# Performance work log

Hardware: AMD Instinct MI355X
Metric: run time of the kernel (lower is better)

Reference implementation:

```python
import jax, jax.numpy as jnp
import numpy as np

SELU_SCALE = 1.0507009873554805
SELU_ALPHA = 1.6732632423543772

def _learned_activation(x, w):
    # softmax-blended mixture of 8 activations plus a zero 'linear' branch
    p = jax.nn.softmax(w)
    sig = jax.nn.sigmoid(x)
    elu = jax.nn.elu(x)
    tanh = jnp.tanh(x)
    relu = jax.nn.relu(x)
    silu = jax.nn.silu(x)
    gelu = jax.nn.gelu(x, approximate=False)
    selu = SELU_SCALE * jnp.where(x > 0, x, SELU_ALPHA * jnp.expm1(x))
    mish = x * jnp.tanh(jax.nn.softplus(x))
    return (p[0] * sig + p[1] * elu + p[2] * tanh + p[3] * relu
            + p[4] * silu + p[5] * gelu + p[6] * selu + p[7] * mish)  # p[8]*0 (linear=0)


def setup_inputs() -> dict:
    key = jax.random.key(0)
    ks = jax.random.split(key, 10)
    B, D, H, E, M = 1024, 1024, 2048, 8, 2048
    init_units = 1024
    s = lambda fan_in: 1.0 / np.sqrt(fan_in)
    x = jax.random.normal(ks[0], (B, D), jnp.float32)
    gate_w = jax.random.normal(ks[1], (D, E), jnp.float32) * s(D)
    expert_w = jax.random.normal(ks[2], (E, D, H), jnp.float32) * s(D)
    expert_b = jnp.zeros((E, H), jnp.float32)
    conn_w1 = jax.random.normal(ks[3], (E, H, 32), jnp.float32) * s(H)
    conn_b1 = jnp.zeros((E, 32), jnp.float32)
    conn_w2 = jax.random.normal(ks[4], (E, 32, H), jnp.float32) * s(32)
    conn_b2 = jnp.zeros((E, H), jnp.float32)
    neuron_avg = jax.random.uniform(ks[5], (E, H), jnp.float32)
    # initial mask: first initial_units neurons active per expert
    neuron_mask = jnp.tile(
        jnp.concatenate([jnp.ones((init_units,), jnp.float32),
                         jnp.zeros((H - init_units,), jnp.float32)])[None, :], (E, 1))
    mem_read_w = jax.random.normal(ks[6], (H, M), jnp.float32) * s(H)
    mem_read_b = jnp.zeros((M,), jnp.float32)
    memory = jax.random.normal(ks[7], (M, H), jnp.float32) * s(M)
    act_w = jnp.ones((9,), jnp.float32)
    return {"x": x, "gate_w": gate_w, "expert_w": expert_w, "expert_b": expert_b,
            "conn_w1": conn_w1, "conn_b1": conn_b1, "conn_w2": conn_w2, "conn_b2": conn_b2,
            "neuron_avg": neuron_avg, "neuron_mask": neuron_mask,
            "mem_read_w": mem_read_w, "mem_read_b": mem_read_b,
            "memory": memory, "act_w": act_w}


def reference(x, gate_w, expert_w, expert_b, conn_w1, conn_b1, conn_w2, conn_b2,
              neuron_avg, neuron_mask, mem_read_w, mem_read_b, memory, act_w):
    # --- MoE gate over experts ---
    gate = jax.nn.softmax(x @ gate_w, axis=-1)  # [B, E]
    # --- DynamicConnectivity soft gating, per expert (from neuron_activation_avg) ---
    h1 = jax.nn.relu(jnp.einsum('eh,ehk->ek', neuron_avg, conn_w1) + conn_b1)  # [E, 32]
    conn = jax.nn.sigmoid(jnp.einsum('ek,ekh->eh', h1, conn_w2) + conn_b2)     # [E, H]
    # --- plastic dense experts: z -> gated -> masked -> relu ---
    z = jnp.einsum('bd,edh->ebh', x, expert_w) + expert_b[:, None, :]  # [E, B, H]
    a = jax.nn.relu(z * (conn * neuron_mask)[:, None, :])              # [E, B, H]
    moe_out = jnp.einsum('be,ebh->bh', gate, a)                        # [B, H]
    # --- episodic memory read (attention over memory slots) ---
    attn = jax.nn.softmax(moe_out @ mem_read_w + mem_read_b, axis=-1)  # [B, M]
    read_vec = attn @ memory                                           # [B, H]
    # --- blended learned activation on residual sum ---
    return _learned_activation(moe_out + read_vec, act_w)
```

## Files before the change

kernel.cpp:

```cpp
#include <hip/hip_runtime.h>
#include <hip/hip_bf16.h>
#include <math.h>

typedef __bf16 bf16_t;
typedef __bf16 bf16x8 __attribute__((ext_vector_type(8)));
typedef float f32x4 __attribute__((ext_vector_type(4)));

#define B_DIM 1024
#define D_DIM 1024
#define H_DIM 2048
#define E_DIM 8
#define M_DIM 2048

typedef const __attribute__((address_space(1))) unsigned int as1_uint;
typedef __attribute__((address_space(3))) unsigned int as3_uint;

__device__ __forceinline__ void gl_lds16(const void* g, void* l) {
  __builtin_amdgcn_global_load_lds((as1_uint*)g, (as3_uint*)l, 16, 0, 0);
}

#define WAITV(n) asm volatile("s_waitcnt vmcnt(" #n ")" ::: "memory")

__global__ __launch_bounds__(256) void cvt_kernel(const float* __restrict__ in,
                                                  bf16_t* __restrict__ out) {
  size_t i = ((size_t)blockIdx.x * 256 + threadIdx.x) * 8;
  float4 a = *(const float4*)&in[i];
  float4 b = *(const float4*)&in[i + 4];
  bf16x8 o;
  o[0] = (bf16_t)a.x; o[1] = (bf16_t)a.y; o[2] = (bf16_t)a.z; o[3] = (bf16_t)a.w;
  o[4] = (bf16_t)b.x; o[5] = (bf16_t)b.y; o[6] = (bf16_t)b.z; o[7] = (bf16_t)b.w;
  *(bf16x8*)&out[i] = o;
}

__global__ __launch_bounds__(256) void transpose_all(
    const float* __restrict__ ew, const float* __restrict__ mrw, const float* __restrict__ mem,
    bf16_t* __restrict__ wbT, bf16_t* __restrict__ mrT, bf16_t* __restrict__ memT) {
  __shared__ float tile[64][65];
  const int z = blockIdx.z;
  const float* in; bf16_t* out; int R, C;
  if (z < 8) {
    if (blockIdx.y >= 16) return;
    in = ew + (size_t)z * D_DIM * H_DIM; out = wbT + (size_t)z * D_DIM * H_DIM;
    R = D_DIM; C = H_DIM;
  } else if (z == 8) {
    in = mrw; out = mrT; R = H_DIM; C = M_DIM;
  } else {
    in = mem; out = memT; R = M_DIM; C = H_DIM;
  }
  int c0 = blockIdx.x * 64, r0 = blockIdx.y * 64;
  int t = threadIdx.x;
  int cq = (t & 15) * 4, rr = t >> 4;
#pragma unroll
  for (int i = 0; i < 4; ++i) {
    int r = rr + 16 * i;
    float4 v = *(const float4*)&in[(size_t)(r0 + r) * C + c0 + cq];
    tile[r][cq] = v.x; tile[r][cq + 1] = v.y; tile[r][cq + 2] = v.z; tile[r][cq + 3] = v.w;
  }
  __syncthreads();
  int r8 = (t & 7) * 8, cc = t >> 3;
#pragma unroll
  for (int i = 0; i < 2; ++i) {
    int c = cc + 32 * i;
    bf16x8 o;
#pragma unroll
    for (int j = 0; j < 8; ++j) o[j] = (bf16_t)tile[r8 + j][c];
    *(bf16x8*)&out[(size_t)(c0 + c) * R + r0 + r8] = o;
  }
}

__global__ __launch_bounds__(256) void gate_kernel(
    const float* __restrict__ x, const float* __restrict__ gw, float* __restrict__ gate_t) {
  __shared__ float red[256][8];
  int b = blockIdx.x, t = threadIdx.x;
  float acc[8] = {0.f, 0.f, 0.f, 0.f, 0.f, 0.f, 0.f, 0.f};
  for (int d = t; d < D_DIM; d += 256) {
    float xv = x[(size_t)b * D_DIM + d];
#pragma unroll
    for (int e = 0; e < 8; ++e) acc[e] += xv * gw[d * 8 + e];
  }
#pragma unroll
  for (int e = 0; e < 8; ++e) red[t][e] = acc[e];
  __syncthreads();
  for (int s = 128; s > 0; s >>= 1) {
    if (t < s) {
#pragma unroll
      for (int e = 0; e < 8; ++e) red[t][e] += red[t + s][e];
    }
    __syncthreads();
  }
  if (t == 0) {
    float m = red[0][0];
#pragma unroll
    for (int e = 1; e < 8; ++e) m = fmaxf(m, red[0][e]);
    float p[8], sum = 0.f;
#pragma unroll
    for (int e = 0; e < 8; ++e) { p[e] = expf(red[0][e] - m); sum += p[e]; }
    float inv = 1.f / sum;
#pragma unroll
    for (int e = 0; e < 8; ++e) gate_t[e * B_DIM + b] = p[e] * inv;
  }
}

__global__ __launch_bounds__(256) void conn1_kernel(
    const float* __restrict__ avg, const float* __restrict__ w1, float* __restrict__ h1p) {
  __shared__ float red[256 * 32];
  int e = blockIdx.x >> 3, c = blockIdx.x & 7, t = threadIdx.x;
  int h = c * 256 + t;
  float av = avg[e * H_DIM + h];
  const float* w1p = &w1[((size_t)e * H_DIM + h) * 32];
#pragma unroll
  for (int k = 0; k < 32; ++k) red[t * 32 + k] = av * w1p[k];
  __syncthreads();
  for (int s = 128; s > 0; s >>= 1) {
    if (t < s) {
#pragma unroll
      for (int k = 0; k < 32; ++k) red[t * 32 + k] += red[(t + s) * 32 + k];
    }
    __syncthreads();
  }
  if (t < 32) h1p[(e * 8 + c) * 32 + t] = red[t];
}

__global__ __launch_bounds__(256) void conn2_kernel(
    const float* __restrict__ h1p, const float* __restrict__ b1,
    const float* __restrict__ w2, const float* __restrict__ b2,
    const float* __restrict__ mask, float* __restrict__ conn) {
  __shared__ float h1[32];
  int e = blockIdx.x >> 3, c = blockIdx.x & 7, t = threadIdx.x;
  if (t < 32) {
    float s = 0.f;
#pragma unroll
    for (int c2 = 0; c2 < 8; ++c2) s += h1p[(e * 8 + c2) * 32 + t];
    h1[t] = fmaxf(s + b1[e * 32 + t], 0.f);
  }
  __syncthreads();
  int h = c * 256 + t;
  float s = b2[e * H_DIM + h];
#pragma unroll
  for (int k = 0; k < 32; ++k) s += h1[k] * w2[((size_t)e * 32 + k) * H_DIM + h];
  conn[e * H_DIM + h] = (1.f / (1.f + expf(-s))) * mask[e * H_DIM + h];
}

__global__ __launch_bounds__(512, 2) void expert_gemm(
    const bf16_t* __restrict__ A, const bf16_t* __restrict__ Bt,
    float* __restrict__ moe, bf16_t* __restrict__ moebf,
    const float* __restrict__ gate_t, const float* __restrict__ conn,
    const float* __restrict__ ebias) {
  __shared__ bf16_t As[2][128 * 64];
  __shared__ bf16_t Bs[8][64 * 64];

  const int wid = (blockIdx.x & 7) * 32 + (blockIdx.x >> 3);
  const int b0 = (wid & 7) * 128;
  const int n0 = (wid >> 3) * 64;

  const int t = threadIdx.x;
  const int lane = t & 63, wave = t >> 6;
  const int wmh = wave >> 2, wnq = wave & 3;
  const int lr = lane & 15, lk = (lane >> 4) * 8;
  const int csw = (lr & 7) << 3;
  const int srow = lane >> 3;
  const int scol = ((lane & 7) ^ srow) << 3;
  const size_t EB = (size_t)H_DIM * D_DIM;

  const bf16_t* Asrc = A + (size_t)(b0 + wave * 16 + srow) * D_DIM + scol;
  const bf16_t* Bsrc = Bt + (size_t)(n0 + wave * 8 + srow) * D_DIM + scol;

  auto stageA = [&](int buf, int kt) {
    gl_lds16(Asrc + (size_t)kt * 64, &As[buf][(wave * 16) * 64]);
    gl_lds16(Asrc + 8 * D_DIM + (size_t)kt * 64, &As[buf][(wave * 16 + 8) * 64]);
  };
  auto stageB = [&](int slot, int e, int kt) {
    gl_lds16(Bsrc + (size_t)e * EB + (size_t)kt * 64, &Bs[slot][(wave * 8) * 64]);
  };
  auto readB = [&](int slot, bf16x8& r0, bf16x8& r1) {
    const bf16_t* Bb = &Bs[slot][0];
    r0 = *(const bf16x8*)&Bb[(wnq * 16 + lr) * 64 + (lk ^ csw)];
    r1 = *(const bf16x8*)&Bb[(wnq * 16 + lr) * 64 + ((32 + lk) ^ csw)];
  };

  f32x4 acc[8][4];
#pragma unroll
  for (int e = 0; e < 8; ++e)
#pragma unroll
    for (int mf = 0; mf < 4; ++mf) acc[e][mf] = (f32x4){0.f, 0.f, 0.f, 0.f};

  stageA(0, 0);
  stageB(0, 0, 0);
  stageB(1, 1, 0);
  stageB(2, 2, 0);
  stageB(3, 3, 0);

  for (int kt = 0; kt < 16; ++kt) {
    const int ab = kt & 1;
    const bool last = (kt == 15);
    bf16x8 af[2][4];
#pragma unroll
    for (int eh = 0; eh < 4; ++eh) {
      const int e0 = eh * 2, e1 = e0 + 1;
      if (eh < 2) {
        stageB(e0 + 4, e0 + 4, kt);
        stageB(e1 + 4, e1 + 4, kt);
      } else if (!last) {
        stageB(e0 - 4, e0 - 4, kt + 1);
        stageB(e1 - 4, e1 - 4, kt + 1);
        if (eh == 2) stageA(ab ^ 1, kt + 1);
      }
      if (eh < 2)        { WAITV(4); }
      else if (!last)    { WAITV(6); }
      else if (eh == 2)  { WAITV(2); }
      else               { WAITV(0); }
      __builtin_amdgcn_s_barrier();
      __builtin_amdgcn_sched_barrier(0);
      if (eh == 0) {
#pragma unroll
        for (int kk = 0; kk < 2; ++kk)
#pragma unroll
          for (int mf = 0; mf < 4; ++mf)
            af[kk][mf] = *(const bf16x8*)&As[ab][(wmh * 64 + mf * 16 + lr) * 64 +
                                                ((kk * 32 + lk) ^ csw)];
      }
      bf16x8 p0, p1, q0, q1;
      readB(e0, p0, p1);
      readB(e1, q0, q1);
      __builtin_amdgcn_s_setprio(1);
#pragma unroll
      for (int mf = 0; mf < 4; ++mf) {
        acc[e0][mf] = __builtin_amdgcn_mfma_f32_16x16x32_bf16(af[0][mf], p0, acc[e0][mf], 0, 0, 0);
        acc[e0][mf] = __builtin_amdgcn_mfma_f32_16x16x32_bf16(af[1][mf], p1, acc[e0][mf], 0, 0, 0);
      }
#pragma unroll
      for (int mf = 0; mf < 4; ++mf) {
        acc[e1][mf] = __builtin_amdgcn_mfma_f32_16x16x32_bf16(af[0][mf], q0, acc[e1][mf], 0, 0, 0);
        acc[e1][mf] = __builtin_amdgcn_mfma_f32_16x16x32_bf16(af[1][mf], q1, acc[e1][mf], 0, 0, 0);
      }
      __builtin_amdgcn_s_setprio(0);
    }
  }

  const int r4 = (lane >> 4) * 4;
  const int gcol = n0 + wnq * 16 + lr;
  const int growb = b0 + wmh * 64;
  f32x4 sum[4];
#pragma unroll
  for (int mf = 0; mf < 4; ++mf) sum[mf] = (f32x4){0.f, 0.f, 0.f, 0.f};
#pragma unroll
  for (int e = 0; e < 8; ++e) {
    const float cm = conn[e * H_DIM + gcol];
    const float bb = ebias[e * H_DIM + gcol];
#pragma unroll
    for (int mf = 0; mf < 4; ++mf) {
      const float4 g4 = *(const float4*)&gate_t[e * B_DIM + growb + mf * 16 + r4];
      sum[mf][0] += fmaxf((acc[e][mf][0] + bb) * cm, 0.f) * g4.x;
      sum[mf][1] += fmaxf((acc[e][mf][1] + bb) * cm, 0.f) * g4.y;
      sum[mf][2] += fmaxf((acc[e][mf][2] + bb) * cm, 0.f) * g4.z;
      sum[mf][3] += fmaxf((acc[e][mf][3] + bb) * cm, 0.f) * g4.w;
    }
  }
#pragma unroll
  for (int mf = 0; mf < 4; ++mf)
#pragma unroll
    for (int j = 0; j < 4; ++j) {
      const int grow = growb + mf * 16 + r4 + j;
      moe[(size_t)grow * H_DIM + gcol] = sum[mf][j];
      moebf[(size_t)grow * H_DIM + gcol] = (bf16_t)sum[mf][j];
    }
}

__global__ __launch_bounds__(512, 2) void gemm_sk4(
    const bf16_t* __restrict__ A, const bf16_t* __restrict__ Bt, float* __restrict__ C) {
  __shared__ bf16_t As[2][128 * 64];
  __shared__ bf16_t Bs[2][128 * 64];

  const int wid = (blockIdx.x & 7) * 64 + (blockIdx.x >> 3);
  const int ez = wid >> 7;
  const int rem = wid & 127;
  const int b0 = (rem & 7) * 128;
  const int n0 = (rem >> 3) * 128;
  const int kbase = ez << 9;

  const int t = threadIdx.x;
  const int lane = t & 63, wave = t >> 6;
  const int wm = wave >> 2, wn = wave & 3;
  const int lr = lane & 15, lk = (lane >> 4) * 8;
  const int csw = (lr & 7) << 3;
  const int srow = lane >> 3;
  const int scol = ((lane & 7) ^ srow) << 3;

  const bf16_t* Arow = A + (size_t)(b0 + srow) * 2048 + kbase + scol;
  const bf16_t* Brow = Bt + (size_t)(n0 + srow) * 2048 + kbase + scol;

  const f32x4 zv = {0.f, 0.f, 0.f, 0.f};
  f32x4 acc[4][2];
#pragma unroll
  for (int mf = 0; mf < 4; ++mf)
#pragma unroll
    for (int nf = 0; nf < 2; ++nf) acc[mf][nf] = zv;

  auto STAGE = [&](int bsel, int kt) {
    const int ko = kt << 6;
#pragma unroll
    for (int i = 0; i < 2; ++i) {
      int rb = i * 64 + wave * 8;
      gl_lds16(Arow + (size_t)rb * 2048 + ko, &As[bsel][rb * 64]);
      gl_lds16(Brow + (size_t)rb * 2048 + ko, &Bs[bsel][rb * 64]);
    }
  };

  auto COMPUTE = [&](int bsel) {
    bf16x8 bfr[2][2];
#pragma unroll
    for (int kk = 0; kk < 2; ++kk)
#pragma unroll
      for (int nf = 0; nf < 2; ++nf)
        bfr[kk][nf] = *(const bf16x8*)&Bs[bsel][(wn * 32 + nf * 16 + lr) * 64 + ((kk * 32 + lk) ^ csw)];
    __builtin_amdgcn_s_setprio(1);
#pragma unroll
    for (int mf = 0; mf < 4; ++mf) {
      bf16x8 a0 = *(const bf16x8*)&As[bsel][(wm * 64 + mf * 16 + lr) * 64 + (lk ^ csw)];
      bf16x8 a1 = *(const bf16x8*)&As[bsel][(wm * 64 + mf * 16 + lr) * 64 + ((32 + lk) ^ csw)];
#pragma unroll
      for (int nf = 0; nf < 2; ++nf)
        acc[mf][nf] = __builtin_amdgcn_mfma_f32_16x16x32_bf16(a0, bfr[0][nf], acc[mf][nf], 0, 0, 0);
#pragma unroll
      for (int nf = 0; nf < 2; ++nf)
        acc[mf][nf] = __builtin_amdgcn_mfma_f32_16x16x32_bf16(a1, bfr[1][nf], acc[mf][nf], 0, 0, 0);
    }
    __builtin_amdgcn_s_setprio(0);
  };

  STAGE(0, 0);
  __syncthreads();
  for (int kt = 0; kt < 7; ++kt) {
    STAGE((kt + 1) & 1, kt + 1);
    COMPUTE(kt & 1);
    __syncthreads();
  }
  COMPUTE(1);

  const int r4 = (lane >> 4) * 4;
#pragma unroll
  for (int mf = 0; mf < 4; ++mf) {
#pragma unroll
    for (int nf = 0; nf < 2; ++nf) {
      int gcol = n0 + wn * 32 + nf * 16 + lr;
#pragma unroll
      for (int j = 0; j < 4; ++j) {
        int grow = b0 + wm * 64 + mf * 16 + r4 + j;
        C[((size_t)ez * B_DIM + grow) * 2048 + gcol] = acc[mf][nf][j];
      }
    }
  }
}

__global__ __launch_bounds__(256) void softmax_kernel(
    const float* __restrict__ lg, const float* __restrict__ bias, bf16_t* __restrict__ attn) {
  const size_t P = (size_t)B_DIM * M_DIM;
  int b = blockIdx.x, t = threadIdx.x;
  int lane = t & 63, wave = t >> 6;
  __shared__ float rmax[4], rsum[4];
  float v[8];
  float m = -1e30f;
#pragma unroll
  for (int i = 0; i < 8; ++i) {
    size_t idx = (size_t)b * M_DIM + i * 256 + t;
    v[i] = lg[idx] + lg[P + idx] + lg[2 * P + idx] + lg[3 * P + idx] + bias[i * 256 + t];
    m = fmaxf(m, v[i]);
  }
#pragma unroll
  for (int off = 32; off >= 1; off >>= 1) m = fmaxf(m, __shfl_xor(m, off));
  if (lane == 0) rmax[wave] = m;
  __syncthreads();
  m = fmaxf(fmaxf(rmax[0], rmax[1]), fmaxf(rmax[2], rmax[3]));
  float s = 0.f;
#pragma unroll
  for (int i = 0; i < 8; ++i) {
    v[i] = __expf(v[i] - m);
    s += v[i];
  }
#pragma unroll
  for (int off = 32; off >= 1; off >>= 1) s += __shfl_xor(s, off);
  if (lane == 0) rsum[wave] = s;
  __syncthreads();
  s = rsum[0] + rsum[1] + rsum[2] + rsum[3];
  float inv = 1.f / s;
#pragma unroll
  for (int i = 0; i < 8; ++i) attn[(size_t)b * M_DIM + i * 256 + t] = (bf16_t)(v[i] * inv);
}

__global__ __launch_bounds__(256) void act_kernel(
    const float* __restrict__ rdv, const float* __restrict__ aw, float* __restrict__ out) {
  const size_t P = (size_t)B_DIM * H_DIM;
  int i = blockIdx.x * 256 + threadIdx.x;
  float w[9], m = -1e30f;
#pragma unroll
  for (int j = 0; j < 9; ++j) { w[j] = aw[j]; m = fmaxf(m, w[j]); }
  float p[9], s = 0.f;
#pragma unroll
  for (int j = 0; j < 9; ++j) { p[j] = expf(w[j] - m); s += p[j]; }
  float inv = 1.f / s;
#pragma unroll
  for (int j = 0; j < 9; ++j) p[j] *= inv;
  float4 mv = ((const float4*)out)[i];
  float4 r0 = ((const float4*)rdv)[i];
  float4 r1 = ((const float4*)(rdv + P))[i];
  float4 r2 = ((const float4*)(rdv + 2 * P))[i];
  float4 r3 = ((const float4*)(rdv + 3 * P))[i];
  float xs[4] = {mv.x + r0.x + r1.x + r2.x + r3.x, mv.y + r0.y + r1.y + r2.y + r3.y,
                 mv.z + r0.z + r1.z + r2.z + r3.z, mv.w + r0.w + r1.w + r2.w + r3.w};
  float os[4];
#pragma unroll
  for (int q = 0; q < 4; ++q) {
    float xv = xs[q];
    float enx = expf(-xv);
    float ex = expf(xv);
    float sig = 1.f / (1.f + enx);
    float em1 = expm1f(xv);
    float th = tanhf(xv);
    float rl = fmaxf(xv, 0.f);
    float si = xv * sig;
    float ge = 0.5f * xv * (1.f + erff(xv * 0.70710678118654752f));
    float se = 1.0507009873554805f * (xv > 0.f ? xv : 1.6732632423543772f * em1);
    float el = xv > 0.f ? xv : em1;
    float sp = log1pf(ex);
    float mi = xv * tanhf(sp);
    os[q] = p[0] * sig + p[1] * el + p[2] * th + p[3] * rl + p[4] * si + p[5] * ge + p[6] * se + p[7] * mi;
  }
  ((float4*)out)[i] = make_float4(os[0], os[1], os[2], os[3]);
}

extern "C" void kernel_launch(void* const* d_in, const int* in_sizes, int n_in,
                              void* d_out, int out_size, void* d_ws, size_t ws_size,
                              hipStream_t stream) {
  const float* x        = (const float*)d_in[0];
  const float* gate_w   = (const float*)d_in[1];
  const float* expert_w = (const float*)d_in[2];
  const float* expert_b = (const float*)d_in[3];
  const float* conn_w1  = (const float*)d_in[4];
  const float* conn_b1  = (const float*)d_in[5];
  const float* conn_w2  = (const float*)d_in[6];
  const float* conn_b2  = (const float*)d_in[7];
  const float* navg     = (const float*)d_in[8];
  const float* nmask    = (const float*)d_in[9];
  const float* mem_rw   = (const float*)d_in[10];
  const float* mem_rb   = (const float*)d_in[11];
  const float* memory   = (const float*)d_in[12];
  const float* act_w    = (const float*)d_in[13];
  float* out = (float*)d_out;

  char* ws = (char*)d_ws;
  bf16_t* wbT    = (bf16_t*)(ws + 0);
  bf16_t* mrT    = (bf16_t*)(ws + 33554432);
  bf16_t* memT   = (bf16_t*)(ws + 41943040);
  float*  gate_t = (float*)(ws + 50331648);
  float*  connb  = (float*)(ws + 50364416);
  bf16_t* x_bf   = (bf16_t*)(ws + 50429952);
  bf16_t* moe_bf = (bf16_t*)(ws + 52527104);
  float*  h1p    = (float*)(ws + 56721408);
  float*  logits = (float*)(ws + 0);
  bf16_t* attn   = (bf16_t*)(ws + 33554432);
  float*  readv  = (float*)(ws + 0);
  float*  moe    = out;

  cvt_kernel<<<dim3(512), 256, 0, stream>>>(x, x_bf);
  transpose_all<<<dim3(32, 32, 10), 256, 0, stream>>>(expert_w, mem_rw, memory, wbT, mrT, memT);
  gate_kernel<<<dim3(B_DIM), 256, 0, stream>>>(x, gate_w, gate_t);
  conn1_kernel<<<dim3(64), 256, 0, stream>>>(navg, conn_w1, h1p);
  conn2_kernel<<<dim3(64), 256, 0, stream>>>(h1p, conn_b1, conn_w2, conn_b2, nmask, connb);
  expert_gemm<<<dim3(256), 512, 0, stream>>>(x_bf, wbT, moe, moe_bf, gate_t, connb, expert_b);
  gemm_sk4<<<dim3(512), 512, 0, stream>>>(moe_bf, mrT, logits);
  softmax_kernel<<<dim3(B_DIM), 256, 0, stream>>>(logits, mem_rb, attn);
  gemm_sk4<<<dim3(512), 512, 0, stream>>>(attn, memT, readv);
  act_kernel<<<dim3((B_DIM * H_DIM) / (256 * 4)), 256, 0, stream>>>(readv, act_w, out);
}
```

Measured before the change: 134.7 us.

## Fuse memory-read GEMM with activation epilogue and enlarge transpose tiles

Replaces the split-K read-vector GEMM, which wrote four partial fp32 slabs, and the separate activation kernel with one GEMM whose epilogue adds the moe residual and applies the blended activation in place. This removes the round trip of the partials through global memory and one launch. The cost is a non-split-K GEMM over K=2048 on 256 blocks, which may have fewer waves in flight. It also makes the transpose kernel use 128x64 tiles on a flat 1D grid.

```diff
diff --git a/kernel.cpp b/kernel.cpp
--- a/kernel.cpp
+++ b/kernel.cpp
@@ -35,32 +35,34 @@
 __global__ __launch_bounds__(256) void transpose_all(
     const float* __restrict__ ew, const float* __restrict__ mrw, const float* __restrict__ mem,
     bf16_t* __restrict__ wbT, bf16_t* __restrict__ mrT, bf16_t* __restrict__ memT) {
-  __shared__ float tile[64][65];
-  const int z = blockIdx.z;
-  const float* in; bf16_t* out; int R, C;
-  if (z < 8) {
-    if (blockIdx.y >= 16) return;
-    in = ew + (size_t)z * D_DIM * H_DIM; out = wbT + (size_t)z * D_DIM * H_DIM;
-    R = D_DIM; C = H_DIM;
-  } else if (z == 8) {
-    in = mrw; out = mrT; R = H_DIM; C = M_DIM;
+  __shared__ float tile[128][65];
+  const int bid = blockIdx.x;
+  const float* in; bf16_t* out; int R, C, rt, ct;
+  if (bid < 2048) {
+    int slab = bid >> 8, rem = bid & 255;
+    in = ew + (size_t)slab * D_DIM * H_DIM; out = wbT + (size_t)slab * D_DIM * H_DIM;
+    R = D_DIM; C = H_DIM; rt = rem >> 5; ct = rem & 31;
+  } else if (bid < 2560) {
+    int rem = bid - 2048;
+    in = mrw; out = mrT; R = H_DIM; C = M_DIM; rt = rem >> 5; ct = rem & 31;
   } else {
-    in = mem; out = memT; R = M_DIM; C = H_DIM;
-  }
-  int c0 = blockIdx.x * 64, r0 = blockIdx.y * 64;
-  int t = threadIdx.x;
+    int rem = bid - 2560;
+    in = mem; out = memT; R = M_DIM; C = H_DIM; rt = rem >> 5; ct = rem & 31;
+  }
+  const int r0 = rt * 128, c0 = ct * 64;
+  const int t = threadIdx.x;
   int cq = (t & 15) * 4, rr = t >> 4;
 #pragma unroll
-  for (int i = 0; i < 4; ++i) {
+  for (int i = 0; i < 8; ++i) {
     int r = rr + 16 * i;
     float4 v = *(const float4*)&in[(size_t)(r0 + r) * C + c0 + cq];
     tile[r][cq] = v.x; tile[r][cq + 1] = v.y; tile[r][cq + 2] = v.z; tile[r][cq + 3] = v.w;
   }
   __syncthreads();
-  int r8 = (t & 7) * 8, cc = t >> 3;
-#pragma unroll
-  for (int i = 0; i < 2; ++i) {
-    int c = cc + 32 * i;
+  int r8 = (t & 15) * 8, cc = t >> 4;
+#pragma unroll
+  for (int i = 0; i < 4; ++i) {
+    int c = cc + 16 * i;
     bf16x8 o;
 #pragma unroll
     for (int j = 0; j < 8; ++j) o[j] = (bf16_t)tile[r8 + j][c];
@@ -387,45 +389,109 @@
   for (int i = 0; i < 8; ++i) attn[(size_t)b * M_DIM + i * 256 + t] = (bf16_t)(v[i] * inv);
 }
 
-__global__ __launch_bounds__(256) void act_kernel(
-    const float* __restrict__ rdv, const float* __restrict__ aw, float* __restrict__ out) {
-  const size_t P = (size_t)B_DIM * H_DIM;
-  int i = blockIdx.x * 256 + threadIdx.x;
-  float w[9], m = -1e30f;
-#pragma unroll
-  for (int j = 0; j < 9; ++j) { w[j] = aw[j]; m = fmaxf(m, w[j]); }
-  float p[9], s = 0.f;
-#pragma unroll
-  for (int j = 0; j < 9; ++j) { p[j] = expf(w[j] - m); s += p[j]; }
-  float inv = 1.f / s;
-#pragma unroll
-  for (int j = 0; j < 9; ++j) p[j] *= inv;
-  float4 mv = ((const float4*)out)[i];
-  float4 r0 = ((const float4*)rdv)[i];
-  float4 r1 = ((const float4*)(rdv + P))[i];
-  float4 r2 = ((const float4*)(rdv + 2 * P))[i];
-  float4 r3 = ((const float4*)(rdv + 3 * P))[i];
-  float xs[4] = {mv.x + r0.x + r1.x + r2.x + r3.x, mv.y + r0.y + r1.y + r2.y + r3.y,
-                 mv.z + r0.z + r1.z + r2.z + r3.z, mv.w + r0.w + r1.w + r2.w + r3.w};
-  float os[4];
-#pragma unroll
-  for (int q = 0; q < 4; ++q) {
-    float xv = xs[q];
-    float enx = expf(-xv);
-    float ex = expf(xv);
-    float sig = 1.f / (1.f + enx);
-    float em1 = expm1f(xv);
-    float th = tanhf(xv);
-    float rl = fmaxf(xv, 0.f);
-    float si = xv * sig;
-    float ge = 0.5f * xv * (1.f + erff(xv * 0.70710678118654752f));
-    float se = 1.0507009873554805f * (xv > 0.f ? xv : 1.6732632423543772f * em1);
-    float el = xv > 0.f ? xv : em1;
-    float sp = log1pf(ex);
-    float mi = xv * tanhf(sp);
-    os[q] = p[0] * sig + p[1] * el + p[2] * th + p[3] * rl + p[4] * si + p[5] * ge + p[6] * se + p[7] * mi;
-  }
-  ((float4*)out)[i] = make_float4(os[0], os[1], os[2], os[3]);
+__global__ __launch_bounds__(512, 2) void gemm_act(
+    const bf16_t* __restrict__ A, const bf16_t* __restrict__ Bt,
+    const float* __restrict__ aw, float* __restrict__ out) {
+  __shared__ bf16_t As[2][64 * 64];
+  __shared__ bf16_t Bs[2][128 * 64];
+
+  const int wid = (blockIdx.x & 7) * 32 + (blockIdx.x >> 3);
+  const int b0 = (wid & 15) * 64;
+  const int n0 = (wid >> 4) * 128;
+
+  const int t = threadIdx.x;
+  const int lane = t & 63, wave = t >> 6;
+  const int wm = wave >> 2, wn = wave & 3;
+  const int lr = lane & 15, lk = (lane >> 4) * 8;
+  const int csw = (lr & 7) << 3;
+  const int srow = lane >> 3;
+  const int scol = ((lane & 7) ^ srow) << 3;
+
+  const bf16_t* Arow = A + (size_t)(b0 + wave * 8 + srow) * M_DIM + scol;
+  const bf16_t* Brow = Bt + (size_t)(n0 + wave * 16 + srow) * M_DIM + scol;
+
+  const f32x4 zv = {0.f, 0.f, 0.f, 0.f};
+  f32x4 acc[2][2];
+#pragma unroll
+  for (int mf = 0; mf < 2; ++mf)
+#pragma unroll
+    for (int nf = 0; nf < 2; ++nf) acc[mf][nf] = zv;
+
+  auto STAGE = [&](int bsel, int kt) {
+    const int ko = kt << 6;
+    gl_lds16(Arow + ko, &As[bsel][(wave * 8) * 64]);
+    gl_lds16(Brow + ko, &Bs[bsel][(wave * 16) * 64]);
+    gl_lds16(Brow + (size_t)8 * M_DIM + ko, &Bs[bsel][(wave * 16 + 8) * 64]);
+  };
+
+  auto COMPUTE = [&](int bsel) {
+    bf16x8 bfr[2][2], afr[2][2];
+#pragma unroll
+    for (int kk = 0; kk < 2; ++kk) {
+#pragma unroll
+      for (int nf = 0; nf < 2; ++nf)
+        bfr[kk][nf] = *(const bf16x8*)&Bs[bsel][(wn * 32 + nf * 16 + lr) * 64 + ((kk * 32 + lk) ^ csw)];
+#pragma unroll
+      for (int mf = 0; mf < 2; ++mf)
+        afr[kk][mf] = *(const bf16x8*)&As[bsel][(wm * 32 + mf * 16 + lr) * 64 + ((kk * 32 + lk) ^ csw)];
+    }
+    __builtin_amdgcn_s_setprio(1);
+#pragma unroll
+    for (int mf = 0; mf < 2; ++mf)
+#pragma unroll
+      for (int nf = 0; nf < 2; ++nf) {
+        acc[mf][nf] = __builtin_amdgcn_mfma_f32_16x16x32_bf16(afr[0][mf], bfr[0][nf], acc[mf][nf], 0, 0, 0);
+        acc[mf][nf] = __builtin_amdgcn_mfma_f32_16x16x32_bf16(afr[1][mf], bfr[1][nf], acc[mf][nf], 0, 0, 0);
+      }
+    __builtin_amdgcn_s_setprio(0);
+  };
+
+  STAGE(0, 0);
+  __syncthreads();
+  for (int kt = 0; kt < 31; ++kt) {
+    STAGE((kt + 1) & 1, kt + 1);
+    COMPUTE(kt & 1);
+    __syncthreads();
+  }
+  COMPUTE(1);
+
+  float w[9], mx = -1e30f;
+#pragma unroll
+  for (int j = 0; j < 9; ++j) { w[j] = aw[j]; mx = fmaxf(mx, w[j]); }
+  float p[9], ps = 0.f;
+#pragma unroll
+  for (int j = 0; j < 9; ++j) { p[j] = expf(w[j] - mx); ps += p[j]; }
+  float pinv = 1.f / ps;
+#pragma unroll
+  for (int j = 0; j < 9; ++j) p[j] *= pinv;
+
+  const int r4 = (lane >> 4) * 4;
+#pragma unroll
+  for (int mf = 0; mf < 2; ++mf) {
+#pragma unroll
+    for (int nf = 0; nf < 2; ++nf) {
+      const int gcol = n0 + wn * 32 + nf * 16 + lr;
+#pragma unroll
+      for (int j = 0; j < 4; ++j) {
+        const int grow = b0 + wm * 32 + mf * 16 + r4 + j;
+        float xv = out[(size_t)grow * H_DIM + gcol] + acc[mf][nf][j];
+        float enx = expf(-xv);
+        float ex = expf(xv);
+        float sig = 1.f / (1.f + enx);
+        float em1 = expm1f(xv);
+        float th = tanhf(xv);
+        float rl = fmaxf(xv, 0.f);
+        float si = xv * sig;
+        float ge = 0.5f * xv * (1.f + erff(xv * 0.70710678118654752f));
+        float se = 1.0507009873554805f * (xv > 0.f ? xv : 1.6732632423543772f * em1);
+        float el = xv > 0.f ? xv : em1;
+        float sp = log1pf(ex);
+        float mi = xv * tanhf(sp);
+        out[(size_t)grow * H_DIM + gcol] =
+            p[0] * sig + p[1] * el + p[2] * th + p[3] * rl + p[4] * si + p[5] * ge + p[6] * se + p[7] * mi;
+      }
+    }
+  }
 }
 
 extern "C" void kernel_launch(void* const* d_in, const int* in_sizes, int n_in,
@@ -458,17 +524,15 @@
   float*  h1p    = (float*)(ws + 56721408);
   float*  logits = (float*)(ws + 0);
   bf16_t* attn   = (bf16_t*)(ws + 33554432);
-  float*  readv  = (float*)(ws + 0);
   float*  moe    = out;
 
   cvt_kernel<<<dim3(512), 256, 0, stream>>>(x, x_bf);
-  transpose_all<<<dim3(32, 32, 10), 256, 0, stream>>>(expert_w, mem_rw, memory, wbT, mrT, memT);
+  transpose_all<<<dim3(3072), 256, 0, stream>>>(expert_w, mem_rw, memory, wbT, mrT, memT);
   gate_kernel<<<dim3(B_DIM), 256, 0, stream>>>(x, gate_w, gate_t);
   conn1_kernel<<<dim3(64), 256, 0, stream>>>(navg, conn_w1, h1p);
   conn2_kernel<<<dim3(64), 256, 0, stream>>>(h1p, conn_b1, conn_w2, conn_b2, nmask, connb);
   expert_gemm<<<dim3(256), 512, 0, stream>>>(x_bf, wbT, moe, moe_bf, gate_t, connb, expert_b);
   gemm_sk4<<<dim3(512), 512, 0, stream>>>(moe_bf, mrT, logits);
   softmax_kernel<<<dim3(B_DIM), 256, 0, stream>>>(logits, mem_rb, attn);
-  gemm_sk4<<<dim3(512), 512, 0, stream>>>(attn, memT, readv);
-  act_kernel<<<dim3((B_DIM * H_DIM) / (256 * 4)), 256, 0, stream>>>(readv, act_w, out);
-}
+  gemm_act<<<dim3(256), 512, 0, stream>>>(attn, memT, act_w, out);
+}
```

After: 140.0 us. 3.9% more time.

## Fuse cvt into gate, merge conn kernels, retile transpose with swizzled LDS

Applied to the files above, without the earlier changes.

Folds the x-to-bf16 conversion into the gate kernel, so x is read once and one launch disappears. Merges the two connectivity kernels into one: each block recomputes the full per-expert h1 reduction, which removes the partial-sum buffer and a launch. The price is eight-fold redundant reads of conn_w1. The weight transpose moves to a 1D grid of 128x64 tiles with an XOR-swizzled LDS layout instead of padding, which also drops the early-exit blocks the old 3D grid wasted on the expert slabs.

```diff
diff --git a/kernel.cpp b/kernel.cpp
--- a/kernel.cpp
+++ b/kernel.cpp
@@ -4,6 +4,7 @@
 
 typedef __bf16 bf16_t;
 typedef __bf16 bf16x8 __attribute__((ext_vector_type(8)));
+typedef __bf16 bf16x4 __attribute__((ext_vector_type(4)));
 typedef float f32x4 __attribute__((ext_vector_type(4)));
 
 #define B_DIM 1024
@@ -21,63 +22,60 @@
 
 #define WAITV(n) asm volatile("s_waitcnt vmcnt(" #n ")" ::: "memory")
 
-__global__ __launch_bounds__(256) void cvt_kernel(const float* __restrict__ in,
-                                                  bf16_t* __restrict__ out) {
-  size_t i = ((size_t)blockIdx.x * 256 + threadIdx.x) * 8;
-  float4 a = *(const float4*)&in[i];
-  float4 b = *(const float4*)&in[i + 4];
-  bf16x8 o;
-  o[0] = (bf16_t)a.x; o[1] = (bf16_t)a.y; o[2] = (bf16_t)a.z; o[3] = (bf16_t)a.w;
-  o[4] = (bf16_t)b.x; o[5] = (bf16_t)b.y; o[6] = (bf16_t)b.z; o[7] = (bf16_t)b.w;
-  *(bf16x8*)&out[i] = o;
-}
-
 __global__ __launch_bounds__(256) void transpose_all(
     const float* __restrict__ ew, const float* __restrict__ mrw, const float* __restrict__ mem,
     bf16_t* __restrict__ wbT, bf16_t* __restrict__ mrT, bf16_t* __restrict__ memT) {
-  __shared__ float tile[64][65];
-  const int z = blockIdx.z;
-  const float* in; bf16_t* out; int R, C;
-  if (z < 8) {
-    if (blockIdx.y >= 16) return;
-    in = ew + (size_t)z * D_DIM * H_DIM; out = wbT + (size_t)z * D_DIM * H_DIM;
-    R = D_DIM; C = H_DIM;
-  } else if (z == 8) {
-    in = mrw; out = mrT; R = H_DIM; C = M_DIM;
+  __shared__ float tile[128 * 64];
+  const int bid = blockIdx.x;
+  const float* in; bf16_t* out; int R, C, rt, ct;
+  if (bid < 2048) {
+    int slab = bid >> 8, rem = bid & 255;
+    in = ew + (size_t)slab * D_DIM * H_DIM; out = wbT + (size_t)slab * D_DIM * H_DIM;
+    R = D_DIM; C = H_DIM; rt = rem >> 5; ct = rem & 31;
+  } else if (bid < 2560) {
+    int rem = bid - 2048;
+    in = mrw; out = mrT; R = H_DIM; C = M_DIM; rt = rem >> 5; ct = rem & 31;
   } else {
-    in = mem; out = memT; R = M_DIM; C = H_DIM;
-  }
-  int c0 = blockIdx.x * 64, r0 = blockIdx.y * 64;
-  int t = threadIdx.x;
+    int rem = bid - 2560;
+    in = mem; out = memT; R = M_DIM; C = H_DIM; rt = rem >> 5; ct = rem & 31;
+  }
+  const int r0 = rt * 128, c0 = ct * 64;
+  const int t = threadIdx.x;
   int cq = (t & 15) * 4, rr = t >> 4;
 #pragma unroll
-  for (int i = 0; i < 4; ++i) {
+  for (int i = 0; i < 8; ++i) {
     int r = rr + 16 * i;
     float4 v = *(const float4*)&in[(size_t)(r0 + r) * C + c0 + cq];
-    tile[r][cq] = v.x; tile[r][cq + 1] = v.y; tile[r][cq + 2] = v.z; tile[r][cq + 3] = v.w;
-  }
-  __syncthreads();
-  int r8 = (t & 7) * 8, cc = t >> 3;
-#pragma unroll
-  for (int i = 0; i < 2; ++i) {
-    int c = cc + 32 * i;
+    float* dst = &tile[r * 64 + (cq ^ (((r >> 3) & 7) << 2))];
+    dst[0] = v.x; dst[1] = v.y; dst[2] = v.z; dst[3] = v.w;
+  }
+  __syncthreads();
+  int r8 = (t & 15) * 8, cc = t >> 4;
+  const int sw = ((t & 15) & 7) << 2;
+#pragma unroll
+  for (int i = 0; i < 4; ++i) {
+    int c = cc + 16 * i;
     bf16x8 o;
 #pragma unroll
-    for (int j = 0; j < 8; ++j) o[j] = (bf16_t)tile[r8 + j][c];
+    for (int j = 0; j < 8; ++j) o[j] = (bf16_t)tile[(r8 + j) * 64 + (c ^ sw)];
     *(bf16x8*)&out[(size_t)(c0 + c) * R + r0 + r8] = o;
   }
 }
 
-__global__ __launch_bounds__(256) void gate_kernel(
-    const float* __restrict__ x, const float* __restrict__ gw, float* __restrict__ gate_t) {
+__global__ __launch_bounds__(256) void gate_cvt_kernel(
+    const float* __restrict__ x, const float* __restrict__ gw,
+    float* __restrict__ gate_t, bf16_t* __restrict__ x_bf) {
   __shared__ float red[256][8];
   int b = blockIdx.x, t = threadIdx.x;
-  float acc[8] = {0.f, 0.f, 0.f, 0.f, 0.f, 0.f, 0.f, 0.f};
-  for (int d = t; d < D_DIM; d += 256) {
-    float xv = x[(size_t)b * D_DIM + d];
-#pragma unroll
-    for (int e = 0; e < 8; ++e) acc[e] += xv * gw[d * 8 + e];
-  }
+  float4 v = ((const float4*)(x + (size_t)b * D_DIM))[t];
+  bf16x4 xb;
+  xb[0] = (bf16_t)v.x; xb[1] = (bf16_t)v.y; xb[2] = (bf16_t)v.z; xb[3] = (bf16_t)v.w;
+  *(bf16x4*)&x_bf[(size_t)b * D_DIM + t * 4] = xb;
+  float acc[8];
+#pragma unroll
+  for (int e = 0; e < 8; ++e)
+    acc[e] = v.x * gw[(4 * t) * 8 + e] + v.y * gw[(4 * t + 1) * 8 + e] +
+             v.z * gw[(4 * t + 2) * 8 + e] + v.w * gw[(4 * t + 3) * 8 + e];
 #pragma unroll
   for (int e = 0; e < 8; ++e) red[t][e] = acc[e];
   __syncthreads();
@@ -101,15 +99,26 @@
   }
 }
 
-__global__ __launch_bounds__(256) void conn1_kernel(
-    const float* __restrict__ avg, const float* __restrict__ w1, float* __restrict__ h1p) {
+__global__ __launch_bounds__(256) void conn_kernel(
+    const float* __restrict__ avg, const float* __restrict__ w1, const float* __restrict__ b1,
+    const float* __restrict__ w2, const float* __restrict__ b2,
+    const float* __restrict__ mask, float* __restrict__ conn) {
   __shared__ float red[256 * 32];
+  __shared__ float h1[32];
   int e = blockIdx.x >> 3, c = blockIdx.x & 7, t = threadIdx.x;
-  int h = c * 256 + t;
-  float av = avg[e * H_DIM + h];
-  const float* w1p = &w1[((size_t)e * H_DIM + h) * 32];
-#pragma unroll
-  for (int k = 0; k < 32; ++k) red[t * 32 + k] = av * w1p[k];
+  float acc[32];
+#pragma unroll
+  for (int k = 0; k < 32; ++k) acc[k] = 0.f;
+#pragma unroll
+  for (int i = 0; i < 8; ++i) {
+    int h = i * 256 + t;
+    float av = avg[e * H_DIM + h];
+    const float* w1p = &w1[((size_t)e * H_DIM + h) * 32];
+#pragma unroll
+    for (int k = 0; k < 32; ++k) acc[k] += av * w1p[k];
+  }
+#pragma unroll
+  for (int k = 0; k < 32; ++k) red[t * 32 + k] = acc[k];
   __syncthreads();
   for (int s = 128; s > 0; s >>= 1) {
     if (t < s) {
@@ -118,21 +127,7 @@
     }
     __syncthreads();
   }
-  if (t < 32) h1p[(e * 8 + c) * 32 + t] = red[t];
-}
-
-__global__ __launch_bounds__(256) void conn2_kernel(
-    const float* __restrict__ h1p, const float* __restrict__ b1,
-    const float* __restrict__ w2, const float* __restrict__ b2,
-    const float* __restrict__ mask, float* __restrict__ conn) {
-  __shared__ float h1[32];
-  int e = blockIdx.x >> 3, c = blockIdx.x & 7, t = threadIdx.x;
-  if (t < 32) {
-    float s = 0.f;
-#pragma unroll
-    for (int c2 = 0; c2 < 8; ++c2) s += h1p[(e * 8 + c2) * 32 + t];
-    h1[t] = fmaxf(s + b1[e * 32 + t], 0.f);
-  }
+  if (t < 32) h1[t] = fmaxf(red[t] + b1[e * 32 + t], 0.f);
   __syncthreads();
   int h = c * 256 + t;
   float s = b2[e * H_DIM + h];
@@ -455,17 +450,14 @@
   float*  connb  = (float*)(ws + 50364416);
   bf16_t* x_bf   = (bf16_t*)(ws + 50429952);
   bf16_t* moe_bf = (bf16_t*)(ws + 52527104);
-  float*  h1p    = (float*)(ws + 56721408);
   float*  logits = (float*)(ws + 0);
   bf16_t* attn   = (bf16_t*)(ws + 33554432);
   float*  readv  = (float*)(ws + 0);
   float*  moe    = out;
 
-  cvt_kernel<<<dim3(512), 256, 0, stream>>>(x, x_bf);
-  transpose_all<<<dim3(32, 32, 10), 256, 0, stream>>>(expert_w, mem_rw, memory, wbT, mrT, memT);
-  gate_kernel<<<dim3(B_DIM), 256, 0, stream>>>(x, gate_w, gate_t);
-  conn1_kernel<<<dim3(64), 256, 0, stream>>>(navg, conn_w1, h1p);
-  conn2_kernel<<<dim3(64), 256, 0, stream>>>(h1p, conn_b1, conn_w2, conn_b2, nmask, connb);
+  transpose_all<<<dim3(3072), 256, 0, stream>>>(expert_w, mem_rw, memory, wbT, mrT, memT);
+  gate_cvt_kernel<<<dim3(B_DIM), 256, 0, stream>>>(x, gate_w, gate_t, x_bf);
+  conn_kernel<<<dim3(64), 256, 0, stream>>>(navg, conn_w1, conn_b1, conn_w2, conn_b2, nmask, connb);
   expert_gemm<<<dim3(256), 512, 0, stream>>>(x_bf, wbT, moe, moe_bf, gate_t, connb, expert_b);
   gemm_sk4<<<dim3(512), 512, 0, stream>>>(moe_bf, mrT, logits);
   softmax_kernel<<<dim3(B_DIM), 256, 0, stream>>>(logits, mem_rb, attn);
```

Measured after the change: 139.2 us. 3.3% more time.
